# Kernel optimization log

Hardware: AMD Instinct MI355X
Metric: run time of the kernel (lower is better)

Reference implementation:

```python
import jax, jax.numpy as jnp
import numpy as np

N = 1024
BATCH = 16384


def setup_inputs() -> dict:
    key = jax.random.key(0)
    k1, k2 = jax.random.split(key)
    log_alpha = jax.random.normal(k1, (BATCH, N), dtype=jnp.float32)
    W = jax.random.normal(k2, (N, N), dtype=jnp.float32)  # unnormalized_transition_matrix
    return {"log_alpha": log_alpha, "W": W}


def reference(log_alpha, W):
    # log_softmax over dim=0 (columns sum to 1 in prob space)
    logT = jax.nn.log_softmax(W, axis=0)  # [N, N]
    # log-domain matmul: out[b, i] = logsumexp_k( logT[i, k] + log_alpha[b, k] )
    # Stable exp-shift trick avoids materializing the [B, N, N] broadcast tensor:
    mA = jnp.max(logT, axis=1, keepdims=True)        # [N, 1] row max of logT
    mB = jnp.max(log_alpha, axis=1, keepdims=True)   # [B, 1] row max of log_alpha
    expA = jnp.exp(logT - mA)                        # [N, N]
    expB = jnp.exp(log_alpha - mB)                   # [B, N]
    s = jnp.einsum('bk,ik->bi', expB, expA)          # [B, N]
    return jnp.log(s) + mB + mA.T                    # [B, N]
```

## Files before the change

### kernel.cpp

```cpp
#include <hip/hip_runtime.h>
#include <hip/hip_bf16.h>
#include <stdint.h>

#define MB_ 16384
#define NN_ 1024
#define KK_ 1024

typedef __bf16 bhalf;
typedef __bf16 bhalf8 __attribute__((ext_vector_type(8)));
typedef __bf16 bhalf4 __attribute__((ext_vector_type(4)));
typedef float f32x4 __attribute__((ext_vector_type(4)));

typedef const __attribute__((address_space(1))) void* gas_ptr;
typedef __attribute__((address_space(3))) void* las_ptr;

__device__ __forceinline__ void gload_lds16(const void* g, void* l) {
  __builtin_amdgcn_global_load_lds((gas_ptr)g, (las_ptr)l, 16, 0, 0);
}

__global__ void k_colpart(const float* __restrict__ W,
                          float* __restrict__ pM, float* __restrict__ pS) {
  int col = blockIdx.x * 256 + threadIdx.x;
  int rc  = blockIdx.y;
  const float* p = W + (size_t)rc * 32 * NN_ + col;
  float v[32];
#pragma unroll
  for (int i = 0; i < 32; ++i) v[i] = p[(size_t)i * NN_];
  float m = v[0];
#pragma unroll
  for (int i = 1; i < 32; ++i) m = fmaxf(m, v[i]);
  float s = 0.f;
#pragma unroll
  for (int i = 0; i < 32; ++i) s += __expf(v[i] - m);
  pM[rc * NN_ + col] = m;
  pS[rc * NN_ + col] = s;
}

__global__ void k_colfin(const float* __restrict__ pM, const float* __restrict__ pS,
                         float* __restrict__ colLSE) {
  int col = blockIdx.x * 256 + threadIdx.x;
  float m = -1e30f;
#pragma unroll
  for (int i = 0; i < 32; ++i) m = fmaxf(m, pM[i * NN_ + col]);
  float s = 0.f;
#pragma unroll
  for (int i = 0; i < 32; ++i) s += pS[i * NN_ + col] * __expf(pM[i * NN_ + col] - m);
  colLSE[col] = m + __logf(s);
}

__global__ void k_expA(const float* __restrict__ W, const float* __restrict__ colLSE,
                       bhalf* __restrict__ eA) {
  int i = blockIdx.x;
  int l = threadIdx.x;
  const float4* row = (const float4*)(W + (size_t)i * NN_);
  const float4* cls = (const float4*)colLSE;
#pragma unroll
  for (int t = 0; t < 4; ++t) {
    float4 wv = row[t * 64 + l];
    float4 cv = cls[t * 64 + l];
    bhalf4 o;
    o[0] = (bhalf)__expf(wv.x - cv.x);
    o[1] = (bhalf)__expf(wv.y - cv.y);
    o[2] = (bhalf)__expf(wv.z - cv.z);
    o[3] = (bhalf)__expf(wv.w - cv.w);
    *(bhalf4*)(eA + (size_t)i * NN_ + t * 256 + l * 4) = o;
  }
}


#define VMW(N)  asm volatile("s_waitcnt vmcnt(" #N ")" ::: "memory")
#define LGKM0   asm volatile("s_waitcnt lgkmcnt(0)" ::: "memory")
#define HINT8   asm volatile("s_waitcnt lgkmcnt(8)" ::: "memory")
#define SBAR    __builtin_amdgcn_s_barrier()
#define SCB0    __builtin_amdgcn_sched_barrier(0)

#define STB(BUF, H, TOFF) do {                                                \
    const bhalf* g_ = pgB + (H) * 131072 + (TOFF) * 64;                       \
    unsigned char* d_ = lds + 65536 + (BUF) * 32768 + (H) * 16384 + tid * 16; \
    gload_lds16(g_, d_); gload_lds16(g_ + 65536, d_ + 8192); } while (0)

#define LOADA(TOFF) do {                                                      \
    _Pragma("unroll")                                                         \
    for (int r_ = 0; r_ < 8; ++r_) va[r_] = pLA4[r_ * 8192 + (TOFF) * 16];    \
  } while (0)

#define CVTA_H(BUF, H) do {                                                   \
    unsigned char* d_ = dA_base + (BUF) * 32768 + (H) * 16384;                \
    _Pragma("unroll")                                                         \
    for (int j_ = 0; j_ < 4; ++j_) {                                          \
      float4 u_ = va[(H) * 4 + j_];                                           \
      bhalf4 o_;                                                              \
      o_[0] = (bhalf)__expf(u_.x); o_[1] = (bhalf)__expf(u_.y);               \
      o_[2] = (bhalf)__expf(u_.z); o_[3] = (bhalf)__expf(u_.w);               \
      *(bhalf4*)(d_ + j_ * 4096) = o_;                                        \
    } } while (0)

#define DS_AF(BUF, Q)                                                         \
  af[0][0] = *(const bhalf8*)(pA0 + (BUF) * 32768 + (Q) * 4096);              \
  af[0][1] = *(const bhalf8*)(pA1 + (BUF) * 32768 + (Q) * 4096);              \
  af[1][0] = *(const bhalf8*)(pA0 + (BUF) * 32768 + (Q) * 4096 + 2048);       \
  af[1][1] = *(const bhalf8*)(pA1 + (BUF) * 32768 + (Q) * 4096 + 2048);

#define DS_BQ(BUF)                                                            \
  _Pragma("unroll")                                                           \
  for (int n_ = 0; n_ < 4; ++n_) {                                            \
    bq[n_][0] = *(const bhalf8*)(pB0 + (BUF) * 32768 + n_ * 2048);            \
    bq[n_][1] = *(const bhalf8*)(pB1 + (BUF) * 32768 + n_ * 2048);            \
  }

#define MFMA8(Q)                                                              \
  __builtin_amdgcn_s_setprio(1);                                              \
  _Pragma("unroll")                                                           \
  for (int m_ = 0; m_ < 2; ++m_)                                              \
    _Pragma("unroll")                                                         \
    for (int n_ = 0; n_ < 4; ++n_)                                            \
      _Pragma("unroll")                                                       \
      for (int kk_ = 0; kk_ < 2; ++kk_)                                       \
        acc[2 * (Q) + m_][n_] = __builtin_amdgcn_mfma_f32_16x16x32_bf16(      \
            af[m_][kk_], bq[n_][kk_], acc[2 * (Q) + m_][n_], 0, 0, 0);        \
  __builtin_amdgcn_s_setprio(0);

#define HEAD  SCB0; SBAR; LGKM0; SCB0

#define KTILE(BUF, LT, BT, VM1, VM2)                                          \
  {                                                                           \
    bhalf8 bq[4][2];                                                          \
    bhalf8 af[2][2];                                                          \
    DS_AF(BUF, 0) DS_BQ(BUF)                                                  \
    if ((LT) >= 0) LOADA(LT);                                                 \
    HINT8;                                                                    \
    HEAD; MFMA8(0) SBAR;                                                      \
    DS_AF(BUF, 1)                                                             \
    if ((BT) >= 0) STB(BUF, 0, BT);                                           \
    HEAD; MFMA8(1)                                                            \
    if ((VM1) == 6) VMW(6); else if ((VM1) == 4) VMW(4);                      \
    else if ((VM1) == 0) VMW(0);                                              \
    if ((LT) >= 0) CVTA_H((BUF) ^ 1, 0);                                      \
    SCB0; SBAR;                                                               \
    DS_AF(BUF, 2)                                                             \
    if ((BT) >= 0) STB(BUF, 1, BT);                                           \
    HEAD; MFMA8(2)                                                            \
    if ((VM2) == 6) VMW(6); else if ((VM2) == 4) VMW(4);                      \
    else if ((VM2) == 0) VMW(0);                                              \
    if ((LT) >= 0) CVTA_H((BUF) ^ 1, 1);                                      \
    SCB0; SBAR;                                                               \
    DS_AF(BUF, 3)                                                             \
    HEAD; MFMA8(3) SBAR;                                                      \
  }

__global__ __launch_bounds__(512, 2) void k_gemm(const float* __restrict__ LA,
                                                 const bhalf* __restrict__ Bt,
                                                 float* __restrict__ out) {
  __shared__ __align__(16) unsigned char lds[131072];

  const int nwg = gridDim.x;
  const int wg  = blockIdx.x;
  const int swz = (wg & 7) * (nwg >> 3) + (wg >> 3);
  const int bm = swz >> 2;
  const int bn = swz & 3;

  const int tid = threadIdx.x;
  const int l = tid & 63;
  const int w = tid >> 6;
  const int wr = w >> 2;
  const int wc = w & 3;

  const int r8  = tid >> 3;
  const int kel = (((tid & 7) ^ (r8 & 7)) << 3);
  const bhalf* pgB = Bt + (size_t)(bn * 256 + r8) * KK_ + kel;

  const float4* pLA4 = (const float4*)(LA + (size_t)(bm * 256 + (tid >> 4)) * KK_) + (tid & 15);
  unsigned char* dA_base = lds + (tid >> 4) * 128 +
                           ((((tid & 15) >> 1) ^ ((tid >> 4) & 7)) << 4) + ((tid & 1) << 3);

  const int kx  = 16 * (l >> 4);
  const int x16 = (l & 7) << 4;
  const int kx0 = kx ^ x16;
  const int kx1 = (64 + kx) ^ x16;
  const unsigned char* pA0 = lds + wr * 16384 + (l & 15) * 128 + kx0;
  const unsigned char* pA1 = lds + wr * 16384 + (l & 15) * 128 + kx1;
  const unsigned char* pB0 = lds + 65536 + (wc >> 1) * 16384 + ((wc & 1) * 64 + (l & 15)) * 128 + kx0;
  const unsigned char* pB1 = lds + 65536 + (wc >> 1) * 16384 + ((wc & 1) * 64 + (l & 15)) * 128 + kx1;

  f32x4 zero = {0.f, 0.f, 0.f, 0.f};
  f32x4 acc[8][4];
#pragma unroll
  for (int m = 0; m < 8; ++m)
#pragma unroll
    for (int n = 0; n < 4; ++n) acc[m][n] = zero;

  float4 va[8];

  LOADA(0);
  STB(0, 0, 0); STB(0, 1, 0);
  STB(1, 0, 1); STB(1, 1, 1);
  VMW(8);
  CVTA_H(0, 0); CVTA_H(0, 1);
  VMW(4);
  LGKM0;
  SBAR;

  for (int p = 0; p < 7; ++p) {
    KTILE(0, 1, 2, 6, 4)
    KTILE(1, 2, 3, 6, 4)
    pLA4 += 32;
    pgB  += 128;
  }
  KTILE(0, 1, -1, 4, 0)
  KTILE(1, -1, -1, -1, -1)

  const int c0 = bn * 256 + wc * 64 + (l & 15);
  const int r0 = bm * 256 + wr * 128 + (l >> 4) * 4;
#pragma unroll
  for (int mf = 0; mf < 8; ++mf) {
#pragma unroll
    for (int r = 0; r < 4; ++r) {
      const int row = r0 + mf * 16 + r;
      float* o = out + (size_t)row * NN_ + c0;
#pragma unroll
      for (int nf = 0; nf < 4; ++nf)
        o[nf * 16] = __logf(acc[mf][nf][r]);
    }
  }
}

extern "C" void kernel_launch(void* const* d_in, const int* in_sizes, int n_in,
                              void* d_out, int out_size, void* d_ws, size_t ws_size,
                              hipStream_t stream) {
  const float* log_alpha = (const float*)d_in[0];
  const float* W         = (const float*)d_in[1];
  float* out = (float*)d_out;

  uintptr_t ws = (uintptr_t)d_ws;
  bhalf* eA     = (bhalf*)(ws);
  float* colLSE = (float*)(ws + 2097152);
  float* pM     = (float*)(ws + 2101248);
  float* pS     = (float*)(ws + 2232320);

  k_colpart<<<dim3(4, 32), 256, 0, stream>>>(W, pM, pS);
  k_colfin<<<4, 256, 0, stream>>>(pM, pS, colLSE);
  k_expA<<<NN_, 64, 0, stream>>>(W, colLSE, eA);
  k_gemm<<<(MB_ / 256) * (NN_ / 256), 512, 0, stream>>>(log_alpha, eA, out);
}
```

Before: 61.47 us.

## Double-buffer A register prefetch to load two K-tiles ahead

Splits the register staging for the fp32 log_alpha tile into two buffers (va0/va1) so global loads for tile k+2 are issued while tile k+1's values are converted to exp/bf16 and written to LDS. The vmcnt waits are retuned so the convert step waits on older loads and the newest load stays in flight across a whole K-tile. This hides global-load latency for the A operand, at the cost of 32 more VGPRs per thread under a 512-thread, 2-wave-per-SIMD launch bound, which risks spills or reduced occupancy.

```diff
diff --git a/kernel.cpp b/kernel.cpp
--- a/kernel.cpp
+++ b/kernel.cpp
@@ -73,22 +73,23 @@
 #define HINT8   asm volatile("s_waitcnt lgkmcnt(8)" ::: "memory")
 #define SBAR    __builtin_amdgcn_s_barrier()
 #define SCB0    __builtin_amdgcn_sched_barrier(0)
+#define NOPS    ((void)0)
 
 #define STB(BUF, H, TOFF) do {                                                \
     const bhalf* g_ = pgB + (H) * 131072 + (TOFF) * 64;                       \
     unsigned char* d_ = lds + 65536 + (BUF) * 32768 + (H) * 16384 + tid * 16; \
     gload_lds16(g_, d_); gload_lds16(g_ + 65536, d_ + 8192); } while (0)
 
-#define LOADA(TOFF) do {                                                      \
+#define LOADA(VA, TOFF) do {                                                  \
     _Pragma("unroll")                                                         \
-    for (int r_ = 0; r_ < 8; ++r_) va[r_] = pLA4[r_ * 8192 + (TOFF) * 16];    \
+    for (int r_ = 0; r_ < 8; ++r_) VA[r_] = pLA4[r_ * 8192 + (TOFF) * 16];    \
   } while (0)
 
-#define CVTA_H(BUF, H) do {                                                   \
+#define CVTA_H(VA, BUF, H) do {                                               \
     unsigned char* d_ = dA_base + (BUF) * 32768 + (H) * 16384;                \
     _Pragma("unroll")                                                         \
     for (int j_ = 0; j_ < 4; ++j_) {                                          \
-      float4 u_ = va[(H) * 4 + j_];                                           \
+      float4 u_ = VA[(H) * 4 + j_];                                           \
       bhalf4 o_;                                                              \
       o_[0] = (bhalf)__expf(u_.x); o_[1] = (bhalf)__expf(u_.y);               \
       o_[2] = (bhalf)__expf(u_.z); o_[3] = (bhalf)__expf(u_.w);               \
@@ -122,30 +123,29 @@
 
 #define HEAD  SCB0; SBAR; LGKM0; SCB0
 
-#define KTILE(BUF, LT, BT, VM1, VM2)                                          \
+#define KTILE(BUF, VAL, VAC, LT, BT, W1, W3, CV)                              \
   {                                                                           \
     bhalf8 bq[4][2];                                                          \
     bhalf8 af[2][2];                                                          \
     DS_AF(BUF, 0) DS_BQ(BUF)                                                  \
-    if ((LT) >= 0) LOADA(LT);                                                 \
+    if ((LT) >= 0) LOADA(VAL, LT);                                            \
     HINT8;                                                                    \
     HEAD; MFMA8(0) SBAR;                                                      \
     DS_AF(BUF, 1)                                                             \
     if ((BT) >= 0) STB(BUF, 0, BT);                                           \
     HEAD; MFMA8(1)                                                            \
-    if ((VM1) == 6) VMW(6); else if ((VM1) == 4) VMW(4);                      \
-    else if ((VM1) == 0) VMW(0);                                              \
-    if ((LT) >= 0) CVTA_H((BUF) ^ 1, 0);                                      \
+    W1;                                                                       \
+    if (CV) CVTA_H(VAC, (BUF) ^ 1, 0);                                        \
     SCB0; SBAR;                                                               \
     DS_AF(BUF, 2)                                                             \
     if ((BT) >= 0) STB(BUF, 1, BT);                                           \
     HEAD; MFMA8(2)                                                            \
-    if ((VM2) == 6) VMW(6); else if ((VM2) == 4) VMW(4);                      \
-    else if ((VM2) == 0) VMW(0);                                              \
-    if ((LT) >= 0) CVTA_H((BUF) ^ 1, 1);                                      \
+    if (CV) CVTA_H(VAC, (BUF) ^ 1, 1);                                        \
     SCB0; SBAR;                                                               \
     DS_AF(BUF, 3)                                                             \
-    HEAD; MFMA8(3) SBAR;                                                      \
+    HEAD; MFMA8(3)                                                            \
+    W3;                                                                       \
+    SCB0; SBAR;                                                               \
   }
 
 __global__ __launch_bounds__(512, 2) void k_gemm(const float* __restrict__ LA,
@@ -189,25 +189,29 @@
 #pragma unroll
     for (int n = 0; n < 4; ++n) acc[m][n] = zero;
 
-  float4 va[8];
-
-  LOADA(0);
+  float4 va0[8], va1[8];
+
+  LOADA(va0, 0);
   STB(0, 0, 0); STB(0, 1, 0);
   STB(1, 0, 1); STB(1, 1, 1);
-  VMW(8);
-  CVTA_H(0, 0); CVTA_H(0, 1);
-  VMW(4);
+  LOADA(va1, 1);
+  VMW(16);
+  CVTA_H(va0, 0, 0); CVTA_H(va0, 0, 1);
+  VMW(12);
   LGKM0;
   SBAR;
 
-  for (int p = 0; p < 7; ++p) {
-    KTILE(0, 1, 2, 6, 4)
-    KTILE(1, 2, 3, 6, 4)
+  KTILE(0, va0, va1, 2, 2, VMW(10), VMW(12), 1)
+
+  for (int p = 0; p < 6; ++p) {
+    KTILE(1, va1, va0, 3, 3, VMW(14), VMW(12), 1)
+    KTILE(0, va0, va1, 4, 4, VMW(14), VMW(12), 1)
     pLA4 += 32;
     pgB  += 128;
   }
-  KTILE(0, 1, -1, 4, 0)
-  KTILE(1, -1, -1, -1, -1)
+  KTILE(1, va1, va0, 3, 3, VMW(14), VMW(12), 1)
+  KTILE(0, va0, va1, -1, -1, VMW(4), VMW(0), 1)
+  KTILE(1, va1, va0, -1, -1, NOPS, NOPS, 0)
 
   const int c0 = bn * 256 + wc * 64 + (l & 15);
   const int r0 = bm * 256 + wr * 128 + (l >> 4) * 4;
```

Result: slower. 89.34 us (+45.3%).
